# Optimization experiments

Hardware: AMD Instinct MI355X
Metric: run time of the kernel (lower is better)

## Reference

```python
import jax, jax.numpy as jnp
import numpy as np

B, S, E, H, NE, K = 4, 1024, 1024, 16, 8, 2
DFF = 4 * E
DH = E // H
EPS = 1e-5


def _ln(x, g, b):
    m = jnp.mean(x, axis=-1, keepdims=True)
    v = jnp.mean(jnp.square(x - m), axis=-1, keepdims=True)
    return (x - m) * jax.lax.rsqrt(v + EPS) * g + b


def setup_inputs() -> dict:
    key = jax.random.key(0)
    ks = jax.random.split(key, 20)
    n = lambda k, sh, s: (jax.random.normal(k, sh, jnp.float32) * s)
    return {
        'x': n(ks[0], (B, S, E), 1.0),
        'ln1_g': jnp.ones((E,), jnp.float32), 'ln1_b': jnp.zeros((E,), jnp.float32),
        'wq': n(ks[1], (E, E), 0.02), 'bq': jnp.zeros((E,), jnp.float32),
        'wk': n(ks[2], (E, E), 0.02), 'bk': jnp.zeros((E,), jnp.float32),
        'wv': n(ks[3], (E, E), 0.02), 'bv': jnp.zeros((E,), jnp.float32),
        'wo': n(ks[4], (E, E), 0.02), 'bo': jnp.zeros((E,), jnp.float32),
        'ln2_g': jnp.ones((E,), jnp.float32), 'ln2_b': jnp.zeros((E,), jnp.float32),
        'sw1': n(ks[5], (E, DFF), 0.02), 'sb1': jnp.zeros((DFF,), jnp.float32),
        'sw2': n(ks[6], (DFF, E), 0.02), 'sb2': jnp.zeros((E,), jnp.float32),
        'ew1': n(ks[7], (NE, E, DFF), 0.02), 'eb1': jnp.zeros((NE, DFF), jnp.float32),
        'ew2': n(ks[8], (NE, DFF, E), 0.02), 'eb2': jnp.zeros((NE, E), jnp.float32),
        'w_gate': n(ks[9], (E, NE), 1.0),
    }


def reference(x, ln1_g, ln1_b, wq, bq, wk, bk, wv, bv, wo, bo,
              ln2_g, ln2_b, sw1, sb1, sw2, sb2, ew1, eb1, ew2, eb2, w_gate):
    # --- self-attention sublayer (eval: no dropout) ---
    res1 = x
    h = _ln(x, ln1_g, ln1_b)
    q = (h @ wq + bq).reshape(B, S, H, DH)
    k = (h @ wk + bk).reshape(B, S, H, DH)
    v = (h @ wv + bv).reshape(B, S, H, DH)
    scores = jnp.einsum('bqhd,bkhd->bhqk', q, k) / jnp.sqrt(jnp.float32(DH))
    attn = jax.nn.softmax(scores, axis=-1)
    ctx = jnp.einsum('bhqk,bkhd->bqhd', attn, v).reshape(B, S, E)
    x = res1 + (ctx @ wo + bo)

    # --- MoE sublayer ---
    res2 = x
    h2 = _ln(x, ln2_g, ln2_b)
    shared = jax.nn.gelu(h2 @ sw1 + sb1, approximate=False) @ sw2 + sb2

    # router (eval: clean logits, no noise)
    logits = h2 @ w_gate                                  # (B,S,NE)
    top_vals, top_idx = jax.lax.top_k(logits, K)          # (B,S,K)
    top_gates = jax.nn.softmax(top_vals, axis=-1)
    onehot = jax.nn.one_hot(top_idx, NE, dtype=x.dtype)   # (B,S,K,NE)
    gates = jnp.einsum('bsk,bske->bse', top_gates, onehot)
    probs = jax.nn.softmax(logits, axis=-1).reshape(-1, NE)
    P = probs.mean(0)
    f = (gates > 0).astype(x.dtype).reshape(-1, NE).mean(0)
    aux_loss = NE * jnp.sum(P * f)

    # dense all-expert compute, gated combine (matches original math)
    eh = jax.nn.gelu(jnp.einsum('bse,neh->bnsh', h2, ew1) + eb1[None, :, None, :],
                     approximate=False)
    eo = jnp.einsum('bnsh,nhe->bnse', eh, ew2) + eb2[None, :, None, :]
    expert_out = jnp.einsum('bnse,bsn->bse', eo, gates)

    return res2 + shared + expert_out, aux_loss
```

## Files before the change

kernel.cpp:

```cpp
#include <hip/hip_runtime.h>
#include <stdint.h>

#define B_    4
#define S_    1024
#define E_    1024
#define H_    16
#define NE_   8
#define DFF_  4096
#define NT_   4096
#define QS_   3072
#define ROWCAP_ 9216

typedef unsigned short u16;
typedef short bf16x8 __attribute__((ext_vector_type(8)));
typedef float f32x4 __attribute__((ext_vector_type(4)));

__device__ __forceinline__ float bf2f(u16 u){ unsigned v = ((unsigned)u) << 16; return __builtin_bit_cast(float, v); }
__device__ __forceinline__ u16 f2bf(float f){ unsigned x = __builtin_bit_cast(unsigned, f); return (u16)((x + 0x7FFFu + ((x >> 16) & 1u)) >> 16); }
__device__ __forceinline__ float gelu_f(float x){ return 0.5f * x * (1.f + erff(x * 0.70710678118f)); }

__device__ __forceinline__ void gl_lds16(const u16* g, u16* l){
  __builtin_amdgcn_global_load_lds((__attribute__((address_space(1))) void*)(const_cast<u16*>(g)),
                                   (__attribute__((address_space(3))) void*)(l), 16, 0, 0);
}

#define KSW32(l)   ((((l) & 3) ^ (((l) >> 3) & 3)) << 3)
#define FRAGOFF(l) (((l) & 15) * 32 + (((((l) >> 4) ^ (((l) >> 1) & 3))) << 3))

__launch_bounds__(256)
__global__ void ln_kernel(const float* __restrict__ x, const float* __restrict__ g,
                          const float* __restrict__ be, u16* __restrict__ out)
{
  const int row = blockIdx.x;
  const float4 v = ((const float4*)(x + (size_t)row * E_))[threadIdx.x];
  float s = v.x + v.y + v.z + v.w;
  #pragma unroll
  for(int mm = 32; mm >= 1; mm >>= 1) s += __shfl_xor(s, mm);
  __shared__ float red[8];
  const int wid = threadIdx.x >> 6;
  if((threadIdx.x & 63) == 0) red[wid] = s;
  __syncthreads();
  const float mean = (red[0] + red[1] + red[2] + red[3]) * (1.0f / E_);
  const float d0 = v.x - mean, d1 = v.y - mean, d2 = v.z - mean, d3 = v.w - mean;
  float q2 = d0*d0 + d1*d1 + d2*d2 + d3*d3;
  #pragma unroll
  for(int mm = 32; mm >= 1; mm >>= 1) q2 += __shfl_xor(q2, mm);
  if((threadIdx.x & 63) == 0) red[4 + wid] = q2;
  __syncthreads();
  const float var = (red[4] + red[5] + red[6] + red[7]) * (1.0f / E_);
  const float rs = rsqrtf(var + 1e-5f);
  const float4 gg = ((const float4*)g)[threadIdx.x];
  const float4 bb = ((const float4*)be)[threadIdx.x];
  ushort4 o;
  o.x = f2bf(d0 * rs * gg.x + bb.x);
  o.y = f2bf(d1 * rs * gg.y + bb.y);
  o.z = f2bf(d2 * rs * gg.z + bb.z);
  o.w = f2bf(d3 * rs * gg.w + bb.w);
  ((ushort4*)(out + (size_t)row * E_))[threadIdx.x] = o;
}

__launch_bounds__(256)
__global__ void transpose_kernel(const float* __restrict__ W, u16* __restrict__ WT, int K, int N)
{
  __shared__ __align__(16) u16 t[64][72];
  const size_t zo = (size_t)blockIdx.z * K * N;
  const int k0 = blockIdx.x * 64, n0 = blockIdx.y * 64;
  const int tid = threadIdx.x;
  const int kr = tid >> 2;
  const int nc = (tid & 3) * 4;
  #pragma unroll
  for(int p = 0; p < 4; p++){
    float4 v = *(const float4*)(W + zo + (size_t)(k0 + kr) * N + n0 + nc + p * 16);
    t[nc + p*16 + 0][kr] = f2bf(v.x);
    t[nc + p*16 + 1][kr] = f2bf(v.y);
    t[nc + p*16 + 2][kr] = f2bf(v.z);
    t[nc + p*16 + 3][kr] = f2bf(v.w);
  }
  __syncthreads();
  const int nr = tid >> 3;
  const int kg = (tid & 7) * 8;
  #pragma unroll
  for(int p = 0; p < 2; p++){
    const int nn = nr + p * 32;
    unsigned u0 = t[nn][kg+0], u1 = t[nn][kg+1], u2 = t[nn][kg+2], u3 = t[nn][kg+3];
    unsigned u4 = t[nn][kg+4], u5 = t[nn][kg+5], u6 = t[nn][kg+6], u7 = t[nn][kg+7];
    uint4 o;
    o.x = u0 | (u1 << 16); o.y = u2 | (u3 << 16); o.z = u4 | (u5 << 16); o.w = u6 | (u7 << 16);
    *(uint4*)(WT + zo + (size_t)(n0 + nn) * K + k0 + kg) = o;
  }
}

__global__ void prep_kernel(const float* __restrict__ bq, const float* __restrict__ bk,
                            const float* __restrict__ bv, float* __restrict__ bcat,
                            int* __restrict__ counts, int* __restrict__ rowlist)
{
  const int i = blockIdx.x * 256 + threadIdx.x;
  if(i < 1024) bcat[i] = bq[i];
  else if(i < 2048) bcat[i] = bk[i - 1024];
  else if(i < 3072) bcat[i] = bv[i - 2048];
  if(i < 16) counts[i] = 0;
  if(i < ROWCAP_) rowlist[i] = -1;
}

template<int MODE>
__launch_bounds__(256)
__global__ void gemm_kernel(const u16* __restrict__ A, const u16* __restrict__ Bt,
                            int N, int Kd, const float* __restrict__ bias,
                            u16* __restrict__ outB)
{
  __shared__ __align__(16) u16 As[2][4096], Bs[2][4096];
  const int tid = threadIdx.x, lane = tid & 63, wid = tid >> 6;
  const int wm = wid >> 1, wn = wid & 1;
  const int tm = blockIdx.y * 128, tn = blockIdx.x * 128;

  const f32x4 zero = {0.f, 0.f, 0.f, 0.f};
  f32x4 acc[4][4];
  #pragma unroll
  for(int m = 0; m < 4; m++)
    #pragma unroll
    for(int n = 0; n < 4; n++) acc[m][n] = zero;

  const int ksw = KSW32(lane);
  const u16* gA0 = A  + (size_t)(tm + wid*32 + (lane >> 2)) * Kd + ksw;
  const u16* gA1 = gA0 + (size_t)16 * Kd;
  const u16* gB0 = Bt + (size_t)(tn + wid*32 + (lane >> 2)) * Kd + ksw;
  const u16* gB1 = gB0 + (size_t)16 * Kd;
  const int seg = wid * 1024;

  const int nt = Kd >> 5;
  gl_lds16(gA0, &As[0][seg]); gl_lds16(gA1, &As[0][seg + 512]);
  gl_lds16(gB0, &Bs[0][seg]); gl_lds16(gB1, &Bs[0][seg + 512]);

  const int fo = FRAGOFF(lane);
  const int fA = wm * 2048, fB = wn * 2048;

  for(int t = 0; t < nt; ++t){
    __syncthreads();
    if(t + 1 < nt){
      const int ko = (t + 1) << 5;
      const int b = (t + 1) & 1;
      gl_lds16(gA0 + ko, &As[b][seg]); gl_lds16(gA1 + ko, &As[b][seg + 512]);
      gl_lds16(gB0 + ko, &Bs[b][seg]); gl_lds16(gB1 + ko, &Bs[b][seg + 512]);
    }
    const u16* as = &As[t & 1][0];
    const u16* bs = &Bs[t & 1][0];
    bf16x8 aF[4], bF[4];
    #pragma unroll
    for(int m = 0; m < 4; m++) aF[m] = *(const bf16x8*)(as + fA + m*512 + fo);
    #pragma unroll
    for(int n = 0; n < 4; n++) bF[n] = *(const bf16x8*)(bs + fB + n*512 + fo);
    #pragma unroll
    for(int m = 0; m < 4; m++)
      #pragma unroll
      for(int n = 0; n < 4; n++)
        acc[m][n] = __builtin_amdgcn_mfma_f32_16x16x32_bf16(aF[m], bF[n], acc[m][n], 0, 0, 0);
  }

  #pragma unroll
  for(int m = 0; m < 4; m++){
    const int row = tm + wm*64 + m*16 + ((lane >> 4) << 2);
    #pragma unroll
    for(int n = 0; n < 4; n++){
      const int col = tn + wn*64 + n*16 + (lane & 15);
      const float bc = bias[col];
      #pragma unroll
      for(int r = 0; r < 4; r++){
        const float v = acc[m][n][r] + bc;
        const size_t idx = (size_t)(row + r) * N + col;
        if constexpr(MODE == 0) outB[idx] = f2bf(v);
        else outB[idx] = f2bf(gelu_f(v));
      }
    }
  }
}

template<int MODE>
__launch_bounds__(256)
__global__ void gemm64_kernel(const u16* __restrict__ A, const u16* __restrict__ Bt,
                              int N, int Kd, const float* __restrict__ bias,
                              float* __restrict__ outF, const float* __restrict__ resid)
{
  __shared__ __align__(16) u16 As[2][2048], Bs[2][4096];
  const int tid = threadIdx.x, lane = tid & 63, wid = tid >> 6;
  const int wm = wid >> 1, wn = wid & 1;
  const int tm = blockIdx.y * 64, tn = blockIdx.x * 128;

  const f32x4 zero = {0.f, 0.f, 0.f, 0.f};
  f32x4 acc[2][4];
  #pragma unroll
  for(int m = 0; m < 2; m++)
    #pragma unroll
    for(int n = 0; n < 4; n++) acc[m][n] = zero;

  const int ksw = KSW32(lane);
  const u16* gA = A + (size_t)(tm + wid*16 + (lane >> 2)) * Kd + ksw;
  const u16* gB0 = Bt + (size_t)(tn + wid*32 + (lane >> 2)) * Kd + ksw;
  const u16* gB1 = gB0 + (size_t)16 * Kd;
  const int segA = wid * 512, segB = wid * 1024;

  const int nt = Kd >> 5;
  gl_lds16(gA, &As[0][segA]);
  gl_lds16(gB0, &Bs[0][segB]); gl_lds16(gB1, &Bs[0][segB + 512]);

  const int fo = FRAGOFF(lane);
  const int fA = wm * 1024, fB = wn * 2048;

  for(int t = 0; t < nt; ++t){
    __syncthreads();
    if(t + 1 < nt){
      const int ko = (t + 1) << 5;
      const int b = (t + 1) & 1;
      gl_lds16(gA + ko, &As[b][segA]);
      gl_lds16(gB0 + ko, &Bs[b][segB]); gl_lds16(gB1 + ko, &Bs[b][segB + 512]);
    }
    const u16* as = &As[t & 1][0];
    const u16* bs = &Bs[t & 1][0];
    bf16x8 aF[2], bF[4];
    #pragma unroll
    for(int m = 0; m < 2; m++) aF[m] = *(const bf16x8*)(as + fA + m*512 + fo);
    #pragma unroll
    for(int n = 0; n < 4; n++) bF[n] = *(const bf16x8*)(bs + fB + n*512 + fo);
    #pragma unroll
    for(int m = 0; m < 2; m++)
      #pragma unroll
      for(int n = 0; n < 4; n++)
        acc[m][n] = __builtin_amdgcn_mfma_f32_16x16x32_bf16(aF[m], bF[n], acc[m][n], 0, 0, 0);
  }

  #pragma unroll
  for(int m = 0; m < 2; m++){
    const int row = tm + wm*32 + m*16 + ((lane >> 4) << 2);
    #pragma unroll
    for(int n = 0; n < 4; n++){
      const int col = tn + wn*64 + n*16 + (lane & 15);
      const float bc = bias[col];
      #pragma unroll
      for(int r = 0; r < 4; r++){
        const float v = acc[m][n][r] + bc;
        const size_t idx = (size_t)(row + r) * N + col;
        if constexpr(MODE == 2) outF[idx] = resid[idx] + v;
        else outF[idx] += v;
      }
    }
  }
}

__launch_bounds__(256)
__global__ void attn_kernel(const u16* __restrict__ qkv, u16* __restrict__ ctx)
{
  __shared__ __align__(16) u16 Ks[64 * 64];
  __shared__ __align__(16) u16 Vt[64 * 72];
  __shared__ __align__(16) u16 Ps[64 * 72];
  const int tid = threadIdx.x, lane = tid & 63, wid = tid >> 6;
  const int bh = blockIdx.y, bb = bh >> 4, hh = bh & 15;
  const int q0 = blockIdx.x * 64;
  const size_t tok0 = (size_t)bb * S_;
  const int hcol = hh * 64;

  bf16x8 aQ0, aQ1;
  {
    const u16* qp = qkv + (tok0 + q0 + wid*16 + (lane & 15)) * QS_ + hcol + ((lane >> 4) << 3);
    aQ0 = *(const bf16x8*)qp;
    aQ1 = *(const bf16x8*)(qp + 32);
  }
  const f32x4 zero = {0.f, 0.f, 0.f, 0.f};
  f32x4 accO[4]; float mrow[4], lrow[4];
  #pragma unroll
  for(int n = 0; n < 4; n++) accO[n] = zero;
  #pragma unroll
  for(int r = 0; r < 4; r++){ mrow[r] = -1e30f; lrow[r] = 0.f; }
  const float sc = 0.125f * 1.44269504f;
  const int ksw8 = (((lane & 7) ^ ((lane >> 3) & 7)) << 3);

  for(int kv0 = 0; kv0 < S_; kv0 += 64){
    __syncthreads();
    {
      const u16* gp = qkv + (tok0 + kv0 + wid*16 + (lane >> 3)) * QS_ + 1024 + hcol + ksw8;
      gl_lds16(gp, Ks + (wid*16) * 64);
      gl_lds16(gp + (size_t)8 * QS_, Ks + (wid*16 + 8) * 64);
    }
    {
      #pragma unroll
      for(int i = 0; i < 2; i++){
        const int tok = (tid >> 3) + i * 32;
        const int d0 = (tid & 7) << 3;
        bf16x8 vv = *(const bf16x8*)(qkv + (tok0 + kv0 + tok) * QS_ + 2048 + hcol + d0);
        #pragma unroll
        for(int j = 0; j < 8; j++) Vt[(d0 + j) * 72 + tok] = (u16)vv[j];
      }
    }
    __syncthreads();
    f32x4 sf[4];
    #pragma unroll
    for(int n = 0; n < 4; n++){
      const int rb = n*16 + (lane & 15);
      bf16x8 b0 = *(const bf16x8*)(Ks + rb*64 + ((((lane >> 4)    ) ^ (lane & 7)) << 3));
      bf16x8 b1 = *(const bf16x8*)(Ks + rb*64 + ((((lane >> 4) + 4) ^ (lane & 7)) << 3));
      f32x4 t = zero;
      t = __builtin_amdgcn_mfma_f32_16x16x32_bf16(aQ0, b0, t, 0, 0, 0);
      t = __builtin_amdgcn_mfma_f32_16x16x32_bf16(aQ1, b1, t, 0, 0, 0);
      sf[n] = t;
    }
    #pragma unroll
    for(int r = 0; r < 4; r++){
      const float s0 = sf[0][r]*sc, s1 = sf[1][r]*sc, s2 = sf[2][r]*sc, s3 = sf[3][r]*sc;
      float mx = fmaxf(fmaxf(s0, s1), fmaxf(s2, s3));
      #pragma unroll
      for(int mm = 1; mm < 16; mm <<= 1) mx = fmaxf(mx, __shfl_xor(mx, mm));
      const float mnew = fmaxf(mrow[r], mx);
      const float resc = exp2f(mrow[r] - mnew);
      mrow[r] = mnew;
      const float p0 = exp2f(s0 - mnew), p1 = exp2f(s1 - mnew);
      const float p2 = exp2f(s2 - mnew), p3 = exp2f(s3 - mnew);
      float ps = p0 + p1 + p2 + p3;
      #pragma unroll
      for(int mm = 1; mm < 16; mm <<= 1) ps += __shfl_xor(ps, mm);
      lrow[r] = lrow[r] * resc + ps;
      #pragma unroll
      for(int n = 0; n < 4; n++) accO[n][r] *= resc;
      const int prow = wid*16 + ((lane >> 4) << 2) + r;
      Ps[prow*72 +      (lane & 15)] = f2bf(p0);
      Ps[prow*72 + 16 + (lane & 15)] = f2bf(p1);
      Ps[prow*72 + 32 + (lane & 15)] = f2bf(p2);
      Ps[prow*72 + 48 + (lane & 15)] = f2bf(p3);
    }
    bf16x8 pa0 = *(const bf16x8*)(Ps + (wid*16 + (lane & 15)) * 72 + ((lane >> 4) << 3));
    bf16x8 pa1 = *(const bf16x8*)(Ps + (wid*16 + (lane & 15)) * 72 + 32 + ((lane >> 4) << 3));
    #pragma unroll
    for(int n = 0; n < 4; n++){
      bf16x8 b0 = *(const bf16x8*)(Vt + (n*16 + (lane & 15)) * 72 + ((lane >> 4) << 3));
      bf16x8 b1 = *(const bf16x8*)(Vt + (n*16 + (lane & 15)) * 72 + 32 + ((lane >> 4) << 3));
      accO[n] = __builtin_amdgcn_mfma_f32_16x16x32_bf16(pa0, b0, accO[n], 0, 0, 0);
      accO[n] = __builtin_amdgcn_mfma_f32_16x16x32_bf16(pa1, b1, accO[n], 0, 0, 0);
    }
  }
  const size_t cbase = tok0 * E_ + hcol;
  #pragma unroll
  for(int n = 0; n < 4; n++)
    #pragma unroll
    for(int r = 0; r < 4; r++){
      const int row = q0 + wid*16 + ((lane >> 4) << 2) + r;
      const int col = n*16 + (lane & 15);
      ctx[cbase + (size_t)row * E_ + col] = f2bf(accO[n][r] / lrow[r]);
    }
}

__launch_bounds__(256)
__global__ void router_kernel(const u16* __restrict__ h2, const float* __restrict__ wg,
                              float* __restrict__ probs, float* __restrict__ tkgate,
                              int* __restrict__ tkidx, int* __restrict__ counts)
{
  const int tok = blockIdx.x * 4 + (threadIdx.x >> 6);
  const int lane = threadIdx.x & 63;
  const u16* hr = h2 + (size_t)tok * E_;
  float a0=0,a1=0,a2=0,a3=0,a4=0,a5=0,a6=0,a7=0;
  for(int i0 = lane * 8; i0 < E_; i0 += 512){
    bf16x8 hv = *(const bf16x8*)(hr + i0);
    #pragma unroll
    for(int j = 0; j < 8; j++){
      const float hx = bf2f((u16)hv[j]);
      const float* wr = wg + (size_t)(i0 + j) * NE_;
      float4 w0 = *(const float4*)wr;
      float4 w1 = *(const float4*)(wr + 4);
      a0 += hx*w0.x; a1 += hx*w0.y; a2 += hx*w0.z; a3 += hx*w0.w;
      a4 += hx*w1.x; a5 += hx*w1.y; a6 += hx*w1.z; a7 += hx*w1.w;
    }
  }
  #pragma unroll
  for(int mm = 1; mm < 64; mm <<= 1){
    a0 += __shfl_xor(a0, mm); a1 += __shfl_xor(a1, mm); a2 += __shfl_xor(a2, mm); a3 += __shfl_xor(a3, mm);
    a4 += __shfl_xor(a4, mm); a5 += __shfl_xor(a5, mm); a6 += __shfl_xor(a6, mm); a7 += __shfl_xor(a7, mm);
  }
  if(lane == 0){
    float lg[8] = {a0,a1,a2,a3,a4,a5,a6,a7};
    float mx = lg[0];
    #pragma unroll
    for(int e = 1; e < 8; e++) mx = fmaxf(mx, lg[e]);
    float se = 0.f, ex[8];
    #pragma unroll
    for(int e = 0; e < 8; e++){ ex[e] = expf(lg[e] - mx); se += ex[e]; }
    const float inv = 1.f / se;
    float* pr = probs + (size_t)tok * 8;
    #pragma unroll
    for(int e = 0; e < 8; e++) pr[e] = ex[e] * inv;
    int i1 = 0; float v1 = lg[0];
    #pragma unroll
    for(int e = 1; e < 8; e++) if(lg[e] > v1){ v1 = lg[e]; i1 = e; }
    int i2 = -1; float v2 = -3.4e38f;
    #pragma unroll
    for(int e = 0; e < 8; e++) if(e != i1 && lg[e] > v2){ v2 = lg[e]; i2 = e; }
    const float t = expf(v2 - v1);
    tkidx[tok*2] = i1; tkidx[tok*2+1] = i2;
    tkgate[tok*2] = 1.f / (1.f + t); tkgate[tok*2+1] = t / (1.f + t);
    atomicAdd(&counts[i1], 1); atomicAdd(&counts[i2], 1);
  }
}

__global__ void scan_kernel(const int* __restrict__ counts, int* __restrict__ aoff, int* __restrict__ cursor)
{
  if(threadIdx.x == 0){
    int o = 0;
    for(int e = 0; e < 8; e++){
      aoff[e] = o; cursor[e] = o;
      o += ((counts[e] + 127) >> 7) << 7;
    }
    aoff[8] = o;
  }
}

__global__ void build_kernel(const int* __restrict__ tkidx, const float* __restrict__ tkgate,
                             int* __restrict__ cursor, int* __restrict__ rowlist, float* __restrict__ rowgate)
{
  const int t = blockIdx.x * 256 + threadIdx.x;
  if(t >= NT_) return;
  #pragma unroll
  for(int kk = 0; kk < 2; kk++){
    const int e = tkidx[t*2 + kk];
    const int pos = atomicAdd(&cursor[e], 1);
    rowlist[pos] = t; rowgate[pos] = tkgate[t*2 + kk];
  }
}

__launch_bounds__(256)
__global__ void egemm1_kernel(const u16* __restrict__ Ah2, const u16* __restrict__ ewT,
                              const float* __restrict__ eb1,
                              const int* __restrict__ rowlist, const int* __restrict__ aoff,
                              u16* __restrict__ ehid)
{
  const int rowTile = blockIdx.y * 128;
  if(rowTile >= aoff[8]) return;
  int e = 0;
  #pragma unroll
  for(int i = 1; i < 8; i++) if(rowTile >= aoff[i]) e = i;
  __shared__ __align__(16) u16 As[2][4096], Bs[2][4096];
  const int tid = threadIdx.x, lane = tid & 63, wid = tid >> 6;
  const int wm = wid >> 1, wn = wid & 1;
  const int tn = blockIdx.x * 128;
  const u16* Bt = ewT + (size_t)e * DFF_ * E_;

  const int r0 = rowTile + wid*32 + (lane >> 2);
  int t0 = rowlist[r0];      if(t0 < 0) t0 = 0;
  int t1 = rowlist[r0 + 16]; if(t1 < 0) t1 = 0;
  const int ksw = KSW32(lane);
  const u16* gA0 = Ah2 + (size_t)t0 * E_ + ksw;
  const u16* gA1 = Ah2 + (size_t)t1 * E_ + ksw;
  const u16* gB0 = Bt + (size_t)(tn + wid*32 + (lane >> 2)) * E_ + ksw;
  const u16* gB1 = gB0 + (size_t)16 * E_;
  const int seg = wid * 1024;

  const f32x4 zero = {0.f,0.f,0.f,0.f};
  f32x4 acc[4][4];
  #pragma unroll
  for(int m = 0; m < 4; m++)
    #pragma unroll
    for(int n = 0; n < 4; n++) acc[m][n] = zero;

  gl_lds16(gA0, &As[0][seg]); gl_lds16(gA1, &As[0][seg + 512]);
  gl_lds16(gB0, &Bs[0][seg]); gl_lds16(gB1, &Bs[0][seg + 512]);

  const int fo = FRAGOFF(lane);
  const int fA = wm * 2048, fB = wn * 2048;
  const int nt = E_ >> 5;

  for(int t = 0; t < nt; ++t){
    __syncthreads();
    if(t + 1 < nt){
      const int ko = (t + 1) << 5;
      const int b = (t + 1) & 1;
      gl_lds16(gA0 + ko, &As[b][seg]); gl_lds16(gA1 + ko, &As[b][seg + 512]);
      gl_lds16(gB0 + ko, &Bs[b][seg]); gl_lds16(gB1 + ko, &Bs[b][seg + 512]);
    }
    const u16* as = &As[t & 1][0];
    const u16* bs = &Bs[t & 1][0];
    bf16x8 aF[4], bF[4];
    #pragma unroll
    for(int m = 0; m < 4; m++) aF[m] = *(const bf16x8*)(as + fA + m*512 + fo);
    #pragma unroll
    for(int n = 0; n < 4; n++) bF[n] = *(const bf16x8*)(bs + fB + n*512 + fo);
    #pragma unroll
    for(int m = 0; m < 4; m++)
      #pragma unroll
      for(int n = 0; n < 4; n++)
        acc[m][n] = __builtin_amdgcn_mfma_f32_16x16x32_bf16(aF[m], bF[n], acc[m][n], 0, 0, 0);
  }
  #pragma unroll
  for(int m = 0; m < 4; m++){
    const int row = rowTile + wm*64 + m*16 + ((lane >> 4) << 2);
    #pragma unroll
    for(int n = 0; n < 4; n++){
      const int col = tn + wn*64 + n*16 + (lane & 15);
      const float bc = eb1[e * DFF_ + col];
      #pragma unroll
      for(int r = 0; r < 4; r++)
        ehid[(size_t)(row + r) * DFF_ + col] = f2bf(gelu_f(acc[m][n][r] + bc));
    }
  }
}

__launch_bounds__(256)
__global__ void egemm2_kernel(const u16* __restrict__ ehid, const u16* __restrict__ ewT2,
                              const float* __restrict__ eb2,
                              const int* __restrict__ rowlist, const float* __restrict__ rowgate,
                              const int* __restrict__ aoff, float* __restrict__ outF)
{
  const int rowTile = blockIdx.y * 64;
  if(rowTile >= aoff[8]) return;
  int e = 0;
  #pragma unroll
  for(int i = 1; i < 8; i++) if(rowTile >= aoff[i]) e = i;
  __shared__ __align__(16) u16 As[2][2048], Bs[2][4096];
  const int tid = threadIdx.x, lane = tid & 63, wid = tid >> 6;
  const int wm = wid >> 1, wn = wid & 1;
  const int tn = blockIdx.x * 128;
  const u16* Bt = ewT2 + (size_t)e * E_ * DFF_;

  const int ksw = KSW32(lane);
  const u16* gA = ehid + (size_t)(rowTile + wid*16 + (lane >> 2)) * DFF_ + ksw;
  const u16* gB0 = Bt + (size_t)(tn + wid*32 + (lane >> 2)) * DFF_ + ksw;
  const u16* gB1 = gB0 + (size_t)16 * DFF_;
  const int segA = wid * 512, segB = wid * 1024;

  const f32x4 zero = {0.f,0.f,0.f,0.f};
  f32x4 acc[2][4];
  #pragma unroll
  for(int m = 0; m < 2; m++)
    #pragma unroll
    for(int n = 0; n < 4; n++) acc[m][n] = zero;

  gl_lds16(gA, &As[0][segA]);
  gl_lds16(gB0, &Bs[0][segB]); gl_lds16(gB1, &Bs[0][segB + 512]);

  const int fo = FRAGOFF(lane);
  const int fA = wm * 1024, fB = wn * 2048;
  const int nt = DFF_ >> 5;

  for(int t = 0; t < nt; ++t){
    __syncthreads();
    if(t + 1 < nt){
      const int ko = (t + 1) << 5;
      const int b = (t + 1) & 1;
      gl_lds16(gA + ko, &As[b][segA]);
      gl_lds16(gB0 + ko, &Bs[b][segB]); gl_lds16(gB1 + ko, &Bs[b][segB + 512]);
    }
    const u16* as = &As[t & 1][0];
    const u16* bs = &Bs[t & 1][0];
    bf16x8 aF[2], bF[4];
    #pragma unroll
    for(int m = 0; m < 2; m++) aF[m] = *(const bf16x8*)(as + fA + m*512 + fo);
    #pragma unroll
    for(int n = 0; n < 4; n++) bF[n] = *(const bf16x8*)(bs + fB + n*512 + fo);
    #pragma unroll
    for(int m = 0; m < 2; m++)
      #pragma unroll
      for(int n = 0; n < 4; n++)
        acc[m][n] = __builtin_amdgcn_mfma_f32_16x16x32_bf16(aF[m], bF[n], acc[m][n], 0, 0, 0);
  }
  #pragma unroll
  for(int m = 0; m < 2; m++){
    const int row = rowTile + wm*32 + m*16 + ((lane >> 4) << 2);
    #pragma unroll
    for(int r = 0; r < 4; r++){
      const int rr = row + r;
      const int tok = rowlist[rr];
      if(tok < 0) continue;
      const float g = rowgate[rr];
      #pragma unroll
      for(int n = 0; n < 4; n++){
        const int col = tn + wn*64 + n*16 + (lane & 15);
        atomicAdd(&outF[(size_t)tok * E_ + col], g * (acc[m][n][r] + eb2[e * E_ + col]));
      }
    }
  }
}

__launch_bounds__(256)
__global__ void aux_kernel(const float* __restrict__ probs, const int* __restrict__ counts,
                           float* __restrict__ outaux)
{
  float a[8];
  #pragma unroll
  for(int e = 0; e < 8; e++) a[e] = 0.f;
  for(int t = threadIdx.x; t < NT_; t += 256){
    const float* p = probs + (size_t)t * 8;
    #pragma unroll
    for(int e = 0; e < 8; e++) a[e] += p[e];
  }
  #pragma unroll
  for(int mm = 1; mm < 64; mm <<= 1)
    #pragma unroll
    for(int e = 0; e < 8; e++) a[e] += __shfl_xor(a[e], mm);
  __shared__ float part[4][8];
  const int wid = threadIdx.x >> 6;
  if((threadIdx.x & 63) == 0)
    for(int e = 0; e < 8; e++) part[wid][e] = a[e];
  __syncthreads();
  if(threadIdx.x == 0){
    float aux = 0.f;
    for(int e = 0; e < 8; e++){
      const float P = (part[0][e] + part[1][e] + part[2][e] + part[3][e]) / (float)NT_;
      const float f = (float)counts[e] / (float)NT_;
      aux += P * f;
    }
    outaux[0] = (float)NE_ * aux;
  }
}

extern "C" void kernel_launch(void* const* d_in, const int* in_sizes, int n_in,
                              void* d_out, int out_size, void* d_ws, size_t ws_size,
                              hipStream_t stream)
{
  (void)in_sizes; (void)n_in; (void)out_size; (void)ws_size;
  const float* x    = (const float*)d_in[0];
  const float* ln1g = (const float*)d_in[1];
  const float* ln1b = (const float*)d_in[2];
  const float* wq   = (const float*)d_in[3];
  const float* bq   = (const float*)d_in[4];
  const float* wk   = (const float*)d_in[5];
  const float* bk   = (const float*)d_in[6];
  const float* wv   = (const float*)d_in[7];
  const float* bv   = (const float*)d_in[8];
  const float* wo   = (const float*)d_in[9];
  const float* bo   = (const float*)d_in[10];
  const float* ln2g = (const float*)d_in[11];
  const float* ln2b = (const float*)d_in[12];
  const float* sw1  = (const float*)d_in[13];
  const float* sb1  = (const float*)d_in[14];
  const float* sw2  = (const float*)d_in[15];
  const float* sb2  = (const float*)d_in[16];
  const float* ew1  = (const float*)d_in[17];
  const float* eb1  = (const float*)d_in[18];
  const float* ew2  = (const float*)d_in[19];
  const float* eb2  = (const float*)d_in[20];
  const float* wgate= (const float*)d_in[21];
  float* out = (float*)d_out;
  char* ws = (char*)d_ws;

  const size_t MB = 1024ull * 1024ull;
  u16* h     = (u16*)(ws + 0);
  u16* h2    = (u16*)(ws + 8*MB);
  u16* wT    = (u16*)(ws + 16*MB);
  char* rt   = ws + 24*MB;
  float* probs   = (float*)(rt);
  float* tkgate  = (float*)(rt + 128*1024);
  int*   tkidx   = (int*)  (rt + 160*1024);
  int*   counts  = (int*)  (rt + 192*1024);
  int*   aoff    = (int*)  (rt + 192*1024 + 64);
  int*   cursor  = (int*)  (rt + 192*1024 + 128);
  int*   rowlist = (int*)  (rt + 256*1024);
  float* rowgate = (float*)(rt + 296*1024);
  float* bcat    = (float*)(rt + 512*1024);
  u16* qkvb  = (u16*)(ws + 32*MB);
  u16* ctx   = (u16*)(ws + 56*MB);
  u16* hidS  = (u16*)(ws + 64*MB);
  u16* ewT   = (u16*)(ws + 32*MB);
  u16* ehid  = (u16*)(ws + 96*MB);

  ln_kernel<<<NT_, 256, 0, stream>>>(x, ln1g, ln1b, h);
  prep_kernel<<<36, 256, 0, stream>>>(bq, bk, bv, bcat, counts, rowlist);
  transpose_kernel<<<dim3(16,16,1), 256, 0, stream>>>(wq, wT,                 E_, E_);
  transpose_kernel<<<dim3(16,16,1), 256, 0, stream>>>(wk, wT + 1024*1024,     E_, E_);
  transpose_kernel<<<dim3(16,16,1), 256, 0, stream>>>(wv, wT + 2*1024*1024,   E_, E_);
  gemm_kernel<0><<<dim3(24,32), 256, 0, stream>>>(h, wT, QS_, E_, bcat, qkvb);
  attn_kernel<<<dim3(16,64), 256, 0, stream>>>(qkvb, ctx);
  transpose_kernel<<<dim3(16,16,1), 256, 0, stream>>>(wo, wT, E_, E_);
  gemm64_kernel<2><<<dim3(8,64), 256, 0, stream>>>(ctx, wT, E_, E_, bo, out, x);

  ln_kernel<<<NT_, 256, 0, stream>>>(out, ln2g, ln2b, h2);
  transpose_kernel<<<dim3(16,64,1), 256, 0, stream>>>(sw1, wT, E_, DFF_);
  gemm_kernel<1><<<dim3(32,32), 256, 0, stream>>>(h2, wT, DFF_, E_, sb1, hidS);
  transpose_kernel<<<dim3(64,16,1), 256, 0, stream>>>(sw2, wT, DFF_, E_);
  gemm64_kernel<3><<<dim3(8,64), 256, 0, stream>>>(hidS, wT, E_, DFF_, sb2, out, nullptr);

  router_kernel<<<1024, 256, 0, stream>>>(h2, wgate, probs, tkgate, tkidx, counts);
  scan_kernel<<<1, 64, 0, stream>>>(counts, aoff, cursor);
  build_kernel<<<16, 256, 0, stream>>>(tkidx, tkgate, cursor, rowlist, rowgate);

  transpose_kernel<<<dim3(16,64,8), 256, 0, stream>>>(ew1, ewT, E_, DFF_);
  egemm1_kernel<<<dim3(32,72), 256, 0, stream>>>(h2, ewT, eb1, rowlist, aoff, ehid);
  transpose_kernel<<<dim3(64,16,8), 256, 0, stream>>>(ew2, ewT, DFF_, E_);
  egemm2_kernel<<<dim3(8,144), 256, 0, stream>>>(ehid, ewT, eb2, rowlist, rowgate, aoff, out);

  aux_kernel<<<1, 256, 0, stream>>>(probs, counts, out + (size_t)NT_ * E_);
}
```

Measured before the change: 845.3 us.

## Triple-buffer LDS in GEMM kernels with explicit vmcnt waits and split barriers

Converts the double-buffered global_load_lds pipeline in the four GEMM kernels (dense 128, dense 64, and both expert GEMMs) into a three-stage ring. Each stage is issued two K-steps ahead, and the wait uses explicit s_waitcnt vmcnt counts so loads stay in flight across the barrier instead of being drained by __syncthreads. The goal is to hide global-memory latency behind the MFMA work. In exchange, LDS use per block rises by half, which can lower occupancy, and correctness now relies on hand-counted vmcnt values.

```diff
diff --git a/kernel.cpp b/kernel.cpp
--- a/kernel.cpp
+++ b/kernel.cpp
@@ -26,6 +26,10 @@
 
 #define KSW32(l)   ((((l) & 3) ^ (((l) >> 3) & 3)) << 3)
 #define FRAGOFF(l) (((l) & 15) * 32 + (((((l) >> 4) ^ (((l) >> 1) & 3))) << 3))
+
+#define VMCNT(n)   asm volatile("s_waitcnt vmcnt(" #n ")" ::: "memory")
+#define BAR_PRE()  do{ __builtin_amdgcn_sched_barrier(0); __builtin_amdgcn_s_barrier(); __builtin_amdgcn_sched_barrier(0); }while(0)
+#define BAR_POST() do{ asm volatile("" ::: "memory"); __builtin_amdgcn_s_barrier(); __builtin_amdgcn_sched_barrier(0); }while(0)
 
 __launch_bounds__(256)
 __global__ void ln_kernel(const float* __restrict__ x, const float* __restrict__ g,
@@ -108,7 +112,7 @@
                             int N, int Kd, const float* __restrict__ bias,
                             u16* __restrict__ outB)
 {
-  __shared__ __align__(16) u16 As[2][4096], Bs[2][4096];
+  __shared__ __align__(16) u16 As[3][4096], Bs[3][4096];
   const int tid = threadIdx.x, lane = tid & 63, wid = tid >> 6;
   const int wm = wid >> 1, wn = wid & 1;
   const int tm = blockIdx.y * 128, tn = blockIdx.x * 128;
@@ -126,24 +130,18 @@
   const u16* gB0 = Bt + (size_t)(tn + wid*32 + (lane >> 2)) * Kd + ksw;
   const u16* gB1 = gB0 + (size_t)16 * Kd;
   const int seg = wid * 1024;
-
-  const int nt = Kd >> 5;
-  gl_lds16(gA0, &As[0][seg]); gl_lds16(gA1, &As[0][seg + 512]);
-  gl_lds16(gB0, &Bs[0][seg]); gl_lds16(gB1, &Bs[0][seg + 512]);
-
   const int fo = FRAGOFF(lane);
   const int fA = wm * 2048, fB = wn * 2048;
-
-  for(int t = 0; t < nt; ++t){
-    __syncthreads();
-    if(t + 1 < nt){
-      const int ko = (t + 1) << 5;
-      const int b = (t + 1) & 1;
-      gl_lds16(gA0 + ko, &As[b][seg]); gl_lds16(gA1 + ko, &As[b][seg + 512]);
-      gl_lds16(gB0 + ko, &Bs[b][seg]); gl_lds16(gB1 + ko, &Bs[b][seg + 512]);
-    }
-    const u16* as = &As[t & 1][0];
-    const u16* bs = &Bs[t & 1][0];
+  const int nt = Kd >> 5;
+
+  auto stage = [&](int t, int cb){
+    const int ko = t << 5;
+    gl_lds16(gA0 + ko, &As[cb][seg]); gl_lds16(gA1 + ko, &As[cb][seg + 512]);
+    gl_lds16(gB0 + ko, &Bs[cb][seg]); gl_lds16(gB1 + ko, &Bs[cb][seg + 512]);
+  };
+  auto compute = [&](int cb){
+    const u16* as = &As[cb][0];
+    const u16* bs = &Bs[cb][0];
     bf16x8 aF[4], bF[4];
     #pragma unroll
     for(int m = 0; m < 4; m++) aF[m] = *(const bf16x8*)(as + fA + m*512 + fo);
@@ -154,7 +152,21 @@
       #pragma unroll
       for(int n = 0; n < 4; n++)
         acc[m][n] = __builtin_amdgcn_mfma_f32_16x16x32_bf16(aF[m], bF[n], acc[m][n], 0, 0, 0);
-  }
+  };
+
+  stage(0, 0); stage(1, 1);
+  int c0 = 0, c1 = 1, c2 = 2;
+  for(int t = 0; t < nt - 2; ++t){
+    stage(t + 2, c2);
+    VMCNT(8);
+    BAR_PRE();
+    compute(c0);
+    BAR_POST();
+    const int tmp = c0; c0 = c1; c1 = c2; c2 = tmp;
+  }
+  VMCNT(4); BAR_PRE(); compute(c0); BAR_POST();
+  { const int tmp = c0; c0 = c1; c1 = c2; c2 = tmp; }
+  VMCNT(0); BAR_PRE(); compute(c0);
 
   #pragma unroll
   for(int m = 0; m < 4; m++){
@@ -180,7 +192,7 @@
                               int N, int Kd, const float* __restrict__ bias,
                               float* __restrict__ outF, const float* __restrict__ resid)
 {
-  __shared__ __align__(16) u16 As[2][2048], Bs[2][4096];
+  __shared__ __align__(16) u16 As[3][2048], Bs[3][4096];
   const int tid = threadIdx.x, lane = tid & 63, wid = tid >> 6;
   const int wm = wid >> 1, wn = wid & 1;
   const int tm = blockIdx.y * 64, tn = blockIdx.x * 128;
@@ -197,24 +209,18 @@
   const u16* gB0 = Bt + (size_t)(tn + wid*32 + (lane >> 2)) * Kd + ksw;
   const u16* gB1 = gB0 + (size_t)16 * Kd;
   const int segA = wid * 512, segB = wid * 1024;
-
-  const int nt = Kd >> 5;
-  gl_lds16(gA, &As[0][segA]);
-  gl_lds16(gB0, &Bs[0][segB]); gl_lds16(gB1, &Bs[0][segB + 512]);
-
   const int fo = FRAGOFF(lane);
   const int fA = wm * 1024, fB = wn * 2048;
-
-  for(int t = 0; t < nt; ++t){
-    __syncthreads();
-    if(t + 1 < nt){
-      const int ko = (t + 1) << 5;
-      const int b = (t + 1) & 1;
-      gl_lds16(gA + ko, &As[b][segA]);
-      gl_lds16(gB0 + ko, &Bs[b][segB]); gl_lds16(gB1 + ko, &Bs[b][segB + 512]);
-    }
-    const u16* as = &As[t & 1][0];
-    const u16* bs = &Bs[t & 1][0];
+  const int nt = Kd >> 5;
+
+  auto stage = [&](int t, int cb){
+    const int ko = t << 5;
+    gl_lds16(gA + ko, &As[cb][segA]);
+    gl_lds16(gB0 + ko, &Bs[cb][segB]); gl_lds16(gB1 + ko, &Bs[cb][segB + 512]);
+  };
+  auto compute = [&](int cb){
+    const u16* as = &As[cb][0];
+    const u16* bs = &Bs[cb][0];
     bf16x8 aF[2], bF[4];
     #pragma unroll
     for(int m = 0; m < 2; m++) aF[m] = *(const bf16x8*)(as + fA + m*512 + fo);
@@ -225,7 +231,21 @@
       #pragma unroll
       for(int n = 0; n < 4; n++)
         acc[m][n] = __builtin_amdgcn_mfma_f32_16x16x32_bf16(aF[m], bF[n], acc[m][n], 0, 0, 0);
-  }
+  };
+
+  stage(0, 0); stage(1, 1);
+  int c0 = 0, c1 = 1, c2 = 2;
+  for(int t = 0; t < nt - 2; ++t){
+    stage(t + 2, c2);
+    VMCNT(6);
+    BAR_PRE();
+    compute(c0);
+    BAR_POST();
+    const int tmp = c0; c0 = c1; c1 = c2; c2 = tmp;
+  }
+  VMCNT(3); BAR_PRE(); compute(c0); BAR_POST();
+  { const int tmp = c0; c0 = c1; c1 = c2; c2 = tmp; }
+  VMCNT(0); BAR_PRE(); compute(c0);
 
   #pragma unroll
   for(int m = 0; m < 2; m++){
@@ -432,7 +452,7 @@
   int e = 0;
   #pragma unroll
   for(int i = 1; i < 8; i++) if(rowTile >= aoff[i]) e = i;
-  __shared__ __align__(16) u16 As[2][4096], Bs[2][4096];
+  __shared__ __align__(16) u16 As[3][4096], Bs[3][4096];
   const int tid = threadIdx.x, lane = tid & 63, wid = tid >> 6;
   const int wm = wid >> 1, wn = wid & 1;
   const int tn = blockIdx.x * 128;
@@ -447,31 +467,25 @@
   const u16* gB0 = Bt + (size_t)(tn + wid*32 + (lane >> 2)) * E_ + ksw;
   const u16* gB1 = gB0 + (size_t)16 * E_;
   const int seg = wid * 1024;
-
-  const f32x4 zero = {0.f,0.f,0.f,0.f};
-  f32x4 acc[4][4];
-  #pragma unroll
-  for(int m = 0; m < 4; m++)
-    #pragma unroll
-    for(int n = 0; n < 4; n++) acc[m][n] = zero;
-
-  gl_lds16(gA0, &As[0][seg]); gl_lds16(gA1, &As[0][seg + 512]);
-  gl_lds16(gB0, &Bs[0][seg]); gl_lds16(gB1, &Bs[0][seg + 512]);
-
   const int fo = FRAGOFF(lane);
   const int fA = wm * 2048, fB = wn * 2048;
   const int nt = E_ >> 5;
 
-  for(int t = 0; t < nt; ++t){
-    __syncthreads();
-    if(t + 1 < nt){
-      const int ko = (t + 1) << 5;
-      const int b = (t + 1) & 1;
-      gl_lds16(gA0 + ko, &As[b][seg]); gl_lds16(gA1 + ko, &As[b][seg + 512]);
-      gl_lds16(gB0 + ko, &Bs[b][seg]); gl_lds16(gB1 + ko, &Bs[b][seg + 512]);
-    }
-    const u16* as = &As[t & 1][0];
-    const u16* bs = &Bs[t & 1][0];
+  const f32x4 zero = {0.f,0.f,0.f,0.f};
+  f32x4 acc[4][4];
+  #pragma unroll
+  for(int m = 0; m < 4; m++)
+    #pragma unroll
+    for(int n = 0; n < 4; n++) acc[m][n] = zero;
+
+  auto stage = [&](int t, int cb){
+    const int ko = t << 5;
+    gl_lds16(gA0 + ko, &As[cb][seg]); gl_lds16(gA1 + ko, &As[cb][seg + 512]);
+    gl_lds16(gB0 + ko, &Bs[cb][seg]); gl_lds16(gB1 + ko, &Bs[cb][seg + 512]);
+  };
+  auto compute = [&](int cb){
+    const u16* as = &As[cb][0];
+    const u16* bs = &Bs[cb][0];
     bf16x8 aF[4], bF[4];
     #pragma unroll
     for(int m = 0; m < 4; m++) aF[m] = *(const bf16x8*)(as + fA + m*512 + fo);
@@ -482,7 +496,22 @@
       #pragma unroll
       for(int n = 0; n < 4; n++)
         acc[m][n] = __builtin_amdgcn_mfma_f32_16x16x32_bf16(aF[m], bF[n], acc[m][n], 0, 0, 0);
-  }
+  };
+
+  stage(0, 0); stage(1, 1);
+  int c0 = 0, c1 = 1, c2 = 2;
+  for(int t = 0; t < nt - 2; ++t){
+    stage(t + 2, c2);
+    VMCNT(8);
+    BAR_PRE();
+    compute(c0);
+    BAR_POST();
+    const int tmp = c0; c0 = c1; c1 = c2; c2 = tmp;
+  }
+  VMCNT(4); BAR_PRE(); compute(c0); BAR_POST();
+  { const int tmp = c0; c0 = c1; c1 = c2; c2 = tmp; }
+  VMCNT(0); BAR_PRE(); compute(c0);
+
   #pragma unroll
   for(int m = 0; m < 4; m++){
     const int row = rowTile + wm*64 + m*16 + ((lane >> 4) << 2);
@@ -508,7 +537,7 @@
   int e = 0;
   #pragma unroll
   for(int i = 1; i < 8; i++) if(rowTile >= aoff[i]) e = i;
-  __shared__ __align__(16) u16 As[2][2048], Bs[2][4096];
+  __shared__ __align__(16) u16 As[3][2048], Bs[3][4096];
   const int tid = threadIdx.x, lane = tid & 63, wid = tid >> 6;
   const int wm = wid >> 1, wn = wid & 1;
   const int tn = blockIdx.x * 128;
@@ -519,31 +548,25 @@
   const u16* gB0 = Bt + (size_t)(tn + wid*32 + (lane >> 2)) * DFF_ + ksw;
   const u16* gB1 = gB0 + (size_t)16 * DFF_;
   const int segA = wid * 512, segB = wid * 1024;
-
-  const f32x4 zero = {0.f,0.f,0.f,0.f};
-  f32x4 acc[2][4];
-  #pragma unroll
-  for(int m = 0; m < 2; m++)
-    #pragma unroll
-    for(int n = 0; n < 4; n++) acc[m][n] = zero;
-
-  gl_lds16(gA, &As[0][segA]);
-  gl_lds16(gB0, &Bs[0][segB]); gl_lds16(gB1, &Bs[0][segB + 512]);
-
   const int fo = FRAGOFF(lane);
   const int fA = wm * 1024, fB = wn * 2048;
   const int nt = DFF_ >> 5;
 
-  for(int t = 0; t < nt; ++t){
-    __syncthreads();
-    if(t + 1 < nt){
-      const int ko = (t + 1) << 5;
-      const int b = (t + 1) & 1;
-      gl_lds16(gA + ko, &As[b][segA]);
-      gl_lds16(gB0 + ko, &Bs[b][segB]); gl_lds16(gB1 + ko, &Bs[b][segB + 512]);
-    }
-    const u16* as = &As[t & 1][0];
-    const u16* bs = &Bs[t & 1][0];
+  const f32x4 zero = {0.f,0.f,0.f,0.f};
+  f32x4 acc[2][4];
+  #pragma unroll
+  for(int m = 0; m < 2; m++)
+    #pragma unroll
+    for(int n = 0; n < 4; n++) acc[m][n] = zero;
+
+  auto stage = [&](int t, int cb){
+    const int ko = t << 5;
+    gl_lds16(gA + ko, &As[cb][segA]);
+    gl_lds16(gB0 + ko, &Bs[cb][segB]); gl_lds16(gB1 + ko, &Bs[cb][segB + 512]);
+  };
+  auto compute = [&](int cb){
+    const u16* as = &As[cb][0];
+    const u16* bs = &Bs[cb][0];
     bf16x8 aF[2], bF[4];
     #pragma unroll
     for(int m = 0; m < 2; m++) aF[m] = *(const bf16x8*)(as + fA + m*512 + fo);
@@ -554,7 +577,22 @@
       #pragma unroll
       for(int n = 0; n < 4; n++)
         acc[m][n] = __builtin_amdgcn_mfma_f32_16x16x32_bf16(aF[m], bF[n], acc[m][n], 0, 0, 0);
-  }
+  };
+
+  stage(0, 0); stage(1, 1);
+  int c0 = 0, c1 = 1, c2 = 2;
+  for(int t = 0; t < nt - 2; ++t){
+    stage(t + 2, c2);
+    VMCNT(6);
+    BAR_PRE();
+    compute(c0);
+    BAR_POST();
+    const int tmp = c0; c0 = c1; c1 = c2; c2 = tmp;
+  }
+  VMCNT(3); BAR_PRE(); compute(c0); BAR_POST();
+  { const int tmp = c0; c0 = c1; c1 = c2; c2 = tmp; }
+  VMCNT(0); BAR_PRE(); compute(c0);
+
   #pragma unroll
   for(int m = 0; m < 2; m++){
     const int row = rowTile + wm*32 + m*16 + ((lane >> 4) << 2);
```

After: 854.9 us. No clear change (+1.1%).
